# Kernel tuning notes

Hardware: AMD Instinct MI355X
Metric: run time of the kernel (lower is better)

## Reference

```python
import jax, jax.numpy as jnp
import numpy as np

STATE_DIM, ACTION_DIM, HIDDEN_DIM = 12, 4, 16  # hidden_dim must equal state_dim+action_dim
LN_EPS = 1e-5


def setup_inputs() -> dict:
    key = jax.random.key(0)
    ks = jax.random.split(key, 12)
    B, T = 8192, 256
    D = STATE_DIM + ACTION_DIM  # 16
    H = HIDDEN_DIM
    s = 1.0 / np.sqrt(D)
    sh = 1.0 / np.sqrt(H)
    return {
        "initial_state": jax.random.normal(ks[0], (B, 1, STATE_DIM), jnp.float32),
        "commands": jax.random.normal(ks[1], (B, T, ACTION_DIM), jnp.float32),
        "ln_gamma": jnp.ones((D,), jnp.float32),
        "ln_beta": jnp.zeros((D,), jnp.float32),
        "W_in": jax.random.uniform(ks[2], (H, D), jnp.float32, -s, s),
        "b_in": jax.random.uniform(ks[3], (H,), jnp.float32, -s, s),
        "W_ih": jax.random.uniform(ks[4], (4 * H, D), jnp.float32, -sh, sh),  # LSTM input_size = D
        "W_hh": jax.random.uniform(ks[5], (4 * H, H), jnp.float32, -sh, sh),
        "b_ih": jax.random.uniform(ks[6], (4 * H,), jnp.float32, -sh, sh),
        "b_hh": jax.random.uniform(ks[7], (4 * H,), jnp.float32, -sh, sh),
        "W_out": jax.random.uniform(ks[8], (STATE_DIM, H), jnp.float32, -sh, sh),
        "b_out": jax.random.uniform(ks[9], (STATE_DIM,), jnp.float32, -sh, sh),
    }


def _normalize_sincos(state, cos_idx, sin_idx):
    sn, cs = state[:, sin_idx], state[:, cos_idx]
    norm = jnp.sqrt(sn * sn + cs * cs) + 1e-8
    return state.at[:, sin_idx].set(sn / norm).at[:, cos_idx].set(cs / norm)


def _forward(initial_state, commands, ln_gamma, ln_beta, W_in, b_in,
             W_ih, W_hh, b_ih, b_hh, W_out, b_out):
    B = initial_state.shape[0]
    H = W_hh.shape[1]
    state0 = initial_state[:, 0, :]  # (B, S)
    h0 = jnp.zeros((B, H), initial_state.dtype)
    c0 = jnp.zeros((B, H), initial_state.dtype)

    def step(carry, cmd_t):
        state, h, c = carry
        x = jnp.concatenate([state, cmd_t], axis=-1)          # (B, D)
        mu = jnp.mean(x, axis=-1, keepdims=True)
        var = jnp.mean((x - mu) ** 2, axis=-1, keepdims=True)
        x = (x - mu) * jax.lax.rsqrt(var + LN_EPS) * ln_gamma + ln_beta
        x = x @ W_in.T + b_in                                  # (B, H)
        gates = x @ W_ih.T + b_ih + h @ W_hh.T + b_hh          # (B, 4H)
        i, f, g, o = jnp.split(gates, 4, axis=-1)
        c = jax.nn.sigmoid(f) * c + jax.nn.sigmoid(i) * jnp.tanh(g)
        h = jax.nn.sigmoid(o) * jnp.tanh(c)
        state = state + h @ W_out.T + b_out                    # (B, S)
        state = _normalize_sincos(state, 1, 2)
        state = _normalize_sincos(state, 3, 4)
        state = _normalize_sincos(state, 5, 6)
        return (state, h, c), state

    _, outs = jax.lax.scan(step, (state0, h0, c0), jnp.swapaxes(commands, 0, 1))
    return jnp.swapaxes(outs, 0, 1)  # (B, T, S)


def reference(initial_state, commands, ln_gamma, ln_beta, W_in, b_in,
              W_ih, W_hh, b_ih, b_hh, W_out, b_out):
    return _forward(initial_state, commands, ln_gamma, ln_beta, W_in, b_in,
                    W_ih, W_hh, b_ih, b_hh, W_out, b_out)
```

## Files before the change

kernel.cpp:

```cpp
#include <hip/hip_runtime.h>

typedef float f32x2 __attribute__((ext_vector_type(2)));
typedef float f32x4 __attribute__((ext_vector_type(4)));
typedef _Float16 h16x2 __attribute__((ext_vector_type(2)));
typedef __fp16 fp16x2_raw __attribute__((ext_vector_type(2)));

#define LOG2E 1.44269504088896340736f

static __device__ __forceinline__ float rcp_fast(float x) { return __builtin_amdgcn_rcpf(x); }

static __device__ __forceinline__ f32x2 mk2(float a, float b) { f32x2 v; v[0] = a; v[1] = b; return v; }

static __device__ __forceinline__ float sigmoid_fast(float x) {
    return rcp_fast(1.0f + __builtin_amdgcn_exp2f(-LOG2E * x));
}

static __device__ __forceinline__ float tanh_fast(float x) {
    float a = __builtin_fabsf(x);
    float t = __builtin_amdgcn_exp2f(-2.0f * LOG2E * a);
    float r = (1.0f - t) * rcp_fast(1.0f + t);
    return __builtin_copysignf(r, x);
}

static __device__ __forceinline__ float fdot2(h16x2 a, h16x2 b, float c) {
#if __has_builtin(__builtin_amdgcn_fdot2)
    return __builtin_amdgcn_fdot2(a, b, c, false);
#else
    return c + (float)(a[0]) * (float)(b[0]) + (float)(a[1]) * (float)(b[1]);
#endif
}

static __device__ __forceinline__ h16x2 pk(float a, float b) {
    fp16x2_raw r = __builtin_amdgcn_cvt_pkrtz(a, b);
    return __builtin_bit_cast(h16x2, r);
}

static __device__ __forceinline__ void load_pairs16(const float* p, f32x2* dst) {
    const f32x4* q4 = (const f32x4*)p;
    f32x4 a = q4[0], b = q4[1], c = q4[2], d = q4[3];
    dst[0] = __builtin_shufflevector(a, a, 0, 1);
    dst[1] = __builtin_shufflevector(a, a, 2, 3);
    dst[2] = __builtin_shufflevector(b, b, 0, 1);
    dst[3] = __builtin_shufflevector(b, b, 2, 3);
    dst[4] = __builtin_shufflevector(c, c, 0, 1);
    dst[5] = __builtin_shufflevector(c, c, 2, 3);
    dst[6] = __builtin_shufflevector(d, d, 0, 1);
    dst[7] = __builtin_shufflevector(d, d, 2, 3);
}

__global__ __launch_bounds__(64, 2) void vm_kernel(
    const float* __restrict__ init_state,
    const float* __restrict__ commands,
    const float* __restrict__ ln_g,
    const float* __restrict__ ln_b,
    const float* __restrict__ W_in,
    const float* __restrict__ b_in,
    const float* __restrict__ W_ih,
    const float* __restrict__ W_hh,
    const float* __restrict__ b_ih,
    const float* __restrict__ b_hh,
    const float* __restrict__ W_out,
    const float* __restrict__ b_out,
    float* __restrict__ out,
    int B, int T)
{
    const int lane = threadIdx.x;
    const int j = lane & 15;
    const int g = lane >> 4;
    const int b = blockIdx.x * 4 + g;
    const int gbase = (lane & 48) << 2;
    const bool is_state = (j < 12);

    f32x2 Wih[4][8], Wh32[4][8];
#pragma unroll
    for (int q = 0; q < 4; ++q) {
        load_pairs16(W_ih + (q * 16 + j) * 16, Wih[q]);
        load_pairs16(W_hh + (q * 16 + j) * 16, Wh32[q]);
    }

    f32x2 Wgx[4][8];
    float binacc[4];
#pragma unroll
    for (int q = 0; q < 4; ++q) {
        binacc[q] = 0.0f;
#pragma unroll
        for (int k2 = 0; k2 < 8; ++k2) Wgx[q][k2] = mk2(0.0f, 0.0f);
    }
#pragma unroll
    for (int m = 0; m < 16; ++m) {
        f32x2 wm[8];
        load_pairs16(W_in + m * 16, wm);
        float bm = b_in[m];
#pragma unroll
        for (int q = 0; q < 4; ++q) {
            float wim = Wih[q][m >> 1][m & 1];
            f32x2 w2 = mk2(wim, wim);
#pragma unroll
            for (int k2 = 0; k2 < 8; ++k2) Wgx[q][k2] += w2 * wm[k2];
            binacc[q] += wim * bm;
        }
    }
    float sg[4], cst[4];
    {
        f32x2 gg2[8], bt2[8];
        load_pairs16(ln_g, gg2);
        load_pairs16(ln_b, bt2);
#pragma unroll
        for (int q = 0; q < 4; ++q) {
            f32x2 ss = mk2(0.0f, 0.0f), cc = mk2(0.0f, 0.0f);
#pragma unroll
            for (int k2 = 0; k2 < 8; ++k2) {
                cc += Wgx[q][k2] * bt2[k2];
                Wgx[q][k2] *= gg2[k2];
                ss += Wgx[q][k2];
            }
            sg[q]  = ss[0] + ss[1];
            cst[q] = cc[0] + cc[1] + binacc[q] + b_ih[q * 16 + j] + b_hh[q * 16 + j];
        }
    }

    h16x2 WgxH[4][8], WhH[4][8];
#pragma unroll
    for (int q = 0; q < 4; ++q)
#pragma unroll
        for (int k2 = 0; k2 < 8; ++k2) {
            WgxH[q][k2] = pk(Wgx[q][k2][0], Wgx[q][k2][1]);
            WhH[q][k2]  = pk(Wh32[q][k2][0], Wh32[q][k2][1]);
        }

    h16x2 WoH[8];
    float bo = 0.0f;
#pragma unroll
    for (int k2 = 0; k2 < 8; ++k2) WoH[k2] = pk(0.0f, 0.0f);
    if (is_state) {
        f32x2 wo32[8];
        load_pairs16(W_out + j * 16, wo32);
#pragma unroll
        for (int k2 = 0; k2 < 8; ++k2) WoH[k2] = pk(wo32[k2][0], wo32[k2][1]);
        bo = b_out[j];
    }

    const h16x2 one2 = pk(1.0f, 1.0f);

    float st = is_state ? init_state[b * 12 + j] : 0.0f;
    float c = 0.0f;
    h16x2 hpk[8];
#pragma unroll
    for (int k2 = 0; k2 < 8; ++k2) hpk[k2] = pk(0.0f, 0.0f);

    const float* cmd_ptr = commands + (size_t)b * T * 4 + (j >= 12 ? j - 12 : 0);
    float* out_ptr = out + (size_t)b * T * 12 + j;
    const bool do_cmd = (j >= 12);

    int pj = j;
    if (j >= 1 && j <= 6) pj = ((j - 1) ^ 1) + 1;
    const int paddr = ((lane & 48) | pj) << 2;
    const bool donorm = (j >= 1 && j <= 6);

#define GATHER16(v, dst)                                                      \
    do {                                                                      \
        int _s = __float_as_int(v);                                           \
        _Pragma("unroll")                                                     \
        for (int _i = 0; _i < 16; ++_i)                                       \
            dst[_i] = __int_as_float(                                         \
                __builtin_amdgcn_ds_bpermute(gbase + (_i << 2), _s));         \
    } while (0)

    float cmd0 = do_cmd ? cmd_ptr[0] : 0.0f;
    h16x2 xpk[8];
    float mu, inv;
    {
        float xv = is_state ? st : cmd0;
        float xg[16];
        GATHER16(xv, xg);
#pragma unroll
        for (int i = 0; i < 8; ++i) xpk[i] = pk(xg[2 * i], xg[2 * i + 1]);
        float s0 = 0.0f, s1 = 0.0f, q0 = 0.0f, q1 = 0.0f;
#pragma unroll
        for (int i = 0; i < 4; ++i) {
            s0 = fdot2(xpk[i], one2, s0);
            s1 = fdot2(xpk[i + 4], one2, s1);
            q0 = fdot2(xpk[i], xpk[i], q0);
            q1 = fdot2(xpk[i + 4], xpk[i + 4], q1);
        }
        mu = (s0 + s1) * 0.0625f;
        float var = (q0 + q1) * 0.0625f - mu * mu;
        inv = __builtin_amdgcn_rsqf(var + 1e-5f);
    }

    float cmdS = do_cmd ? cmd_ptr[(size_t)(T > 1 ? 1 : 0) * 4] : 0.0f;
    float cmdN = do_cmd ? cmd_ptr[(size_t)(T > 2 ? 2 : 0) * 4] : 0.0f;

    for (int t = 0; t < T; ++t) {
        float gx[4], gh[4];
#pragma unroll
        for (int q = 0; q < 4; ++q) {
            float a0 = 0.0f, a1 = 0.0f, h0 = 0.0f, h1 = 0.0f;
#pragma unroll
            for (int k = 0; k < 4; ++k) {
                a0 = fdot2(WgxH[q][k], xpk[k], a0);
                a1 = fdot2(WgxH[q][k + 4], xpk[k + 4], a1);
                h0 = fdot2(WhH[q][k], hpk[k], h0);
                h1 = fdot2(WhH[q][k + 4], hpk[k + 4], h1);
            }
            gx[q] = a0 + a1;
            gh[q] = h0 + h1;
        }
        float nmi = -mu * inv;
        float gi = __builtin_fmaf(gx[0], inv, __builtin_fmaf(nmi, sg[0], cst[0] + gh[0]));
        float gf = __builtin_fmaf(gx[1], inv, __builtin_fmaf(nmi, sg[1], cst[1] + gh[1]));
        float gG = __builtin_fmaf(gx[2], inv, __builtin_fmaf(nmi, sg[2], cst[2] + gh[2]));
        float go = __builtin_fmaf(gx[3], inv, __builtin_fmaf(nmi, sg[3], cst[3] + gh[3]));

        float iv = sigmoid_fast(gi);
        float fv = sigmoid_fast(gf);
        float gv = tanh_fast(gG);
        float ov = sigmoid_fast(go);
        c = fv * c + iv * gv;
        float hv = ov * tanh_fast(c);

        {
            float hg[16];
            GATHER16(hv, hg);
#pragma unroll
            for (int i = 0; i < 8; ++i) hpk[i] = pk(hg[2 * i], hg[2 * i + 1]);
        }

        float o0 = 0.0f, o1 = 0.0f;
#pragma unroll
        for (int k = 0; k < 4; ++k) {
            o0 = fdot2(WoH[k], hpk[k], o0);
            o1 = fdot2(WoH[k + 4], hpk[k + 4], o1);
        }
        float st_raw = st + (o0 + o1) + bo;

        float pv = __int_as_float(
            __builtin_amdgcn_ds_bpermute(paddr, __float_as_int(st_raw)));
        float nrm = __builtin_amdgcn_sqrtf(st_raw * st_raw + pv * pv) + 1e-8f;
        float stn = st_raw * rcp_fast(nrm);
        st = donorm ? stn : st_raw;
        if (is_state) out_ptr[0] = st;
        out_ptr += 12;

        {
            float xv = is_state ? st : cmdS;
            float xg[16];
            GATHER16(xv, xg);
#pragma unroll
            for (int i = 0; i < 8; ++i) xpk[i] = pk(xg[2 * i], xg[2 * i + 1]);
        }
        float s0 = 0.0f, s1 = 0.0f, q0 = 0.0f, q1 = 0.0f;
#pragma unroll
        for (int i = 0; i < 4; ++i) {
            s0 = fdot2(xpk[i], one2, s0);
            s1 = fdot2(xpk[i + 4], one2, s1);
            q0 = fdot2(xpk[i], xpk[i], q0);
            q1 = fdot2(xpk[i + 4], xpk[i + 4], q1);
        }
        mu = (s0 + s1) * 0.0625f;
        float var = (q0 + q1) * 0.0625f - mu * mu;
        inv = __builtin_amdgcn_rsqf(var + 1e-5f);

        cmdS = cmdN;
        int tn = t + 3;
        if (tn > T - 1) tn = T - 1;
        if (do_cmd) cmdN = cmd_ptr[(size_t)tn * 4];
    }
#undef GATHER16
}

extern "C" void kernel_launch(void* const* d_in, const int* in_sizes, int n_in,
                              void* d_out, int out_size, void* d_ws, size_t ws_size,
                              hipStream_t stream) {
    const float* init_state = (const float*)d_in[0];
    const float* commands   = (const float*)d_in[1];
    const float* ln_g       = (const float*)d_in[2];
    const float* ln_b       = (const float*)d_in[3];
    const float* W_in       = (const float*)d_in[4];
    const float* b_in       = (const float*)d_in[5];
    const float* W_ih       = (const float*)d_in[6];
    const float* W_hh       = (const float*)d_in[7];
    const float* b_ih       = (const float*)d_in[8];
    const float* b_hh       = (const float*)d_in[9];
    const float* W_out      = (const float*)d_in[10];
    const float* b_out      = (const float*)d_in[11];

    int B = in_sizes[0] / 12;
    int T = in_sizes[1] / (B * 4);

    int blocks = B / 4;
    vm_kernel<<<blocks, 64, 0, stream>>>(init_state, commands, ln_g, ln_b,
                                         W_in, b_in, W_ih, W_hh, b_ih, b_hh,
                                         W_out, b_out, (float*)d_out, B, T);
}
```

Before: 393.1 us.

## Replicate state update across lanes to drop second per-step gather

```diff
diff --git a/kernel.cpp b/kernel.cpp
--- a/kernel.cpp
+++ b/kernel.cpp
@@ -48,7 +48,7 @@
     dst[7] = __builtin_shufflevector(d, d, 2, 3);
 }
 
-__global__ __launch_bounds__(64, 2) void vm_kernel(
+__global__ __launch_bounds__(64, 1) void vm_kernel(
     const float* __restrict__ init_state,
     const float* __restrict__ commands,
     const float* __restrict__ ln_g,
@@ -69,7 +69,6 @@
     const int g = lane >> 4;
     const int b = blockIdx.x * 4 + g;
     const int gbase = (lane & 48) << 2;
-    const bool is_state = (j < 12);
 
     f32x2 Wih[4][8], Wh32[4][8];
 #pragma unroll
@@ -128,34 +127,35 @@
             WhH[q][k2]  = pk(Wh32[q][k2][0], Wh32[q][k2][1]);
         }
 
-    h16x2 WoH[8];
-    float bo = 0.0f;
-#pragma unroll
-    for (int k2 = 0; k2 < 8; ++k2) WoH[k2] = pk(0.0f, 0.0f);
-    if (is_state) {
+    h16x2 WoF[12][8];
+    float boF[12];
+#pragma unroll
+    for (int i = 0; i < 12; ++i) {
         f32x2 wo32[8];
-        load_pairs16(W_out + j * 16, wo32);
-#pragma unroll
-        for (int k2 = 0; k2 < 8; ++k2) WoH[k2] = pk(wo32[k2][0], wo32[k2][1]);
-        bo = b_out[j];
+        load_pairs16(W_out + i * 16, wo32);
+#pragma unroll
+        for (int k2 = 0; k2 < 8; ++k2) WoF[i][k2] = pk(wo32[k2][0], wo32[k2][1]);
+        boF[i] = b_out[i];
     }
 
     const h16x2 one2 = pk(1.0f, 1.0f);
 
-    float st = is_state ? init_state[b * 12 + j] : 0.0f;
+    float st[12];
+    {
+        const f32x4* isp = (const f32x4*)(init_state + b * 12);
+        f32x4 s0 = isp[0], s1 = isp[1], s2 = isp[2];
+#pragma unroll
+        for (int i = 0; i < 4; ++i) {
+            st[i] = s0[i]; st[4 + i] = s1[i]; st[8 + i] = s2[i];
+        }
+    }
     float c = 0.0f;
     h16x2 hpk[8];
 #pragma unroll
     for (int k2 = 0; k2 < 8; ++k2) hpk[k2] = pk(0.0f, 0.0f);
 
-    const float* cmd_ptr = commands + (size_t)b * T * 4 + (j >= 12 ? j - 12 : 0);
-    float* out_ptr = out + (size_t)b * T * 12 + j;
-    const bool do_cmd = (j >= 12);
-
-    int pj = j;
-    if (j >= 1 && j <= 6) pj = ((j - 1) ^ 1) + 1;
-    const int paddr = ((lane & 48) | pj) << 2;
-    const bool donorm = (j >= 1 && j <= 6);
+    const f32x4* cmd4 = (const f32x4*)(commands + (size_t)b * T * 4);
+    float* outp = out + (size_t)b * T * 12 + j * 4;
 
 #define GATHER16(v, dst)                                                      \
     do {                                                                      \
@@ -166,15 +166,19 @@
                 __builtin_amdgcn_ds_bpermute(gbase + (_i << 2), _s));         \
     } while (0)
 
-    float cmd0 = do_cmd ? cmd_ptr[0] : 0.0f;
+#define PACK_X(xpk, cv)                                                       \
+    do {                                                                      \
+        xpk[0] = pk(st[0], st[1]);  xpk[1] = pk(st[2], st[3]);                \
+        xpk[2] = pk(st[4], st[5]);  xpk[3] = pk(st[6], st[7]);                \
+        xpk[4] = pk(st[8], st[9]);  xpk[5] = pk(st[10], st[11]);              \
+        xpk[6] = pk(cv[0], cv[1]);  xpk[7] = pk(cv[2], cv[3]);                \
+    } while (0)
+
     h16x2 xpk[8];
     float mu, inv;
     {
-        float xv = is_state ? st : cmd0;
-        float xg[16];
-        GATHER16(xv, xg);
-#pragma unroll
-        for (int i = 0; i < 8; ++i) xpk[i] = pk(xg[2 * i], xg[2 * i + 1]);
+        f32x4 cmd0 = cmd4[0];
+        PACK_X(xpk, cmd0);
         float s0 = 0.0f, s1 = 0.0f, q0 = 0.0f, q1 = 0.0f;
 #pragma unroll
         for (int i = 0; i < 4; ++i) {
@@ -188,8 +192,8 @@
         inv = __builtin_amdgcn_rsqf(var + 1e-5f);
     }
 
-    float cmdS = do_cmd ? cmd_ptr[(size_t)(T > 1 ? 1 : 0) * 4] : 0.0f;
-    float cmdN = do_cmd ? cmd_ptr[(size_t)(T > 2 ? 2 : 0) * 4] : 0.0f;
+    f32x4 cmdS = cmd4[T > 1 ? 1 : 0];
+    f32x4 cmdN = cmd4[T > 2 ? 2 : 0];
 
     for (int t = 0; t < T; ++t) {
         float gx[4], gh[4];
@@ -226,29 +230,35 @@
             for (int i = 0; i < 8; ++i) hpk[i] = pk(hg[2 * i], hg[2 * i + 1]);
         }
 
-        float o0 = 0.0f, o1 = 0.0f;
-#pragma unroll
-        for (int k = 0; k < 4; ++k) {
-            o0 = fdot2(WoH[k], hpk[k], o0);
-            o1 = fdot2(WoH[k + 4], hpk[k + 4], o1);
-        }
-        float st_raw = st + (o0 + o1) + bo;
-
-        float pv = __int_as_float(
-            __builtin_amdgcn_ds_bpermute(paddr, __float_as_int(st_raw)));
-        float nrm = __builtin_amdgcn_sqrtf(st_raw * st_raw + pv * pv) + 1e-8f;
-        float stn = st_raw * rcp_fast(nrm);
-        st = donorm ? stn : st_raw;
-        if (is_state) out_ptr[0] = st;
-        out_ptr += 12;
+#pragma unroll
+        for (int i = 0; i < 12; ++i) {
+            float d0 = 0.0f, d1 = 0.0f;
+#pragma unroll
+            for (int k = 0; k < 4; ++k) {
+                d0 = fdot2(WoF[i][k], hpk[k], d0);
+                d1 = fdot2(WoF[i][k + 4], hpk[k + 4], d1);
+            }
+            st[i] = st[i] + (d0 + d1) + boF[i];
+        }
+
+#pragma unroll
+        for (int p = 0; p < 3; ++p) {
+            float a = st[1 + 2 * p], bq = st[2 + 2 * p];
+            float r = rcp_fast(__builtin_amdgcn_sqrtf(a * a + bq * bq) + 1e-8f);
+            st[1 + 2 * p] = a * r; st[2 + 2 * p] = bq * r;
+        }
 
         {
-            float xv = is_state ? st : cmdS;
-            float xg[16];
-            GATHER16(xv, xg);
-#pragma unroll
-            for (int i = 0; i < 8; ++i) xpk[i] = pk(xg[2 * i], xg[2 * i + 1]);
-        }
+            f32x4 v0, v1, v2;
+#pragma unroll
+            for (int i = 0; i < 4; ++i) { v0[i] = st[i]; v1[i] = st[4 + i]; v2[i] = st[8 + i]; }
+            f32x4 w = (j == 1) ? v1 : v0;
+            w = (j == 2) ? v2 : w;
+            if (j < 3) *(f32x4*)outp = w;
+            outp += 12;
+        }
+
+        PACK_X(xpk, cmdS);
         float s0 = 0.0f, s1 = 0.0f, q0 = 0.0f, q1 = 0.0f;
 #pragma unroll
         for (int i = 0; i < 4; ++i) {
@@ -264,9 +274,10 @@
         cmdS = cmdN;
         int tn = t + 3;
         if (tn > T - 1) tn = T - 1;
-        if (do_cmd) cmdN = cmd_ptr[(size_t)tn * 4];
+        cmdN = cmd4[tn];
     }
 #undef GATHER16
+#undef PACK_X
 }
 
 extern "C" void kernel_launch(void* const* d_in, const int* in_sizes, int n_in,
```

After: 502.0 us. 27.7% more time.

## Interleave two independent LSTM recurrences per lane and pack hidden-state gathers

Applied to the files above, without the earlier changes.

```diff
diff --git a/kernel.cpp b/kernel.cpp
--- a/kernel.cpp
+++ b/kernel.cpp
@@ -33,6 +33,11 @@
 static __device__ __forceinline__ h16x2 pk(float a, float b) {
     fp16x2_raw r = __builtin_amdgcn_cvt_pkrtz(a, b);
     return __builtin_bit_cast(h16x2, r);
+}
+
+template <int CTRL>
+static __device__ __forceinline__ int dppi(int src) {
+    return __builtin_amdgcn_update_dpp(0, src, CTRL, 0xF, 0xF, true);
 }
 
 static __device__ __forceinline__ void load_pairs16(const float* p, f32x2* dst) {
@@ -48,7 +53,7 @@
     dst[7] = __builtin_shufflevector(d, d, 2, 3);
 }
 
-__global__ __launch_bounds__(64, 2) void vm_kernel(
+__global__ __launch_bounds__(64, 1) void vm_kernel(
     const float* __restrict__ init_state,
     const float* __restrict__ commands,
     const float* __restrict__ ln_g,
@@ -67,9 +72,11 @@
     const int lane = threadIdx.x;
     const int j = lane & 15;
     const int g = lane >> 4;
-    const int b = blockIdx.x * 4 + g;
     const int gbase = (lane & 48) << 2;
     const bool is_state = (j < 12);
+    const int bbase = blockIdx.x * 4;
+    const int bA = bbase + (g & 1);
+    const int bB = bbase + 2 + (g & 1);
 
     f32x2 Wih[4][8], Wh32[4][8];
 #pragma unroll
@@ -140,133 +147,166 @@
         bo = b_out[j];
     }
 
+#define PINH(x) do { int _t = __builtin_bit_cast(int, x); \
+    asm volatile("" : "+v"(_t)); x = __builtin_bit_cast(h16x2, _t); } while (0)
+#define PINF(x) asm volatile("" : "+v"(x))
+#pragma unroll
+    for (int q = 0; q < 4; ++q) {
+#pragma unroll
+        for (int k2 = 0; k2 < 8; ++k2) { PINH(WgxH[q][k2]); PINH(WhH[q][k2]); }
+        PINF(sg[q]); PINF(cst[q]);
+    }
+#pragma unroll
+    for (int k2 = 0; k2 < 8; ++k2) PINH(WoH[k2]);
+    PINF(bo);
+
     const h16x2 one2 = pk(1.0f, 1.0f);
-
-    float st = is_state ? init_state[b * 12 + j] : 0.0f;
-    float c = 0.0f;
-    h16x2 hpk[8];
-#pragma unroll
-    for (int k2 = 0; k2 < 8; ++k2) hpk[k2] = pk(0.0f, 0.0f);
-
-    const float* cmd_ptr = commands + (size_t)b * T * 4 + (j >= 12 ? j - 12 : 0);
-    float* out_ptr = out + (size_t)b * T * 12 + j;
-    const bool do_cmd = (j >= 12);
 
     int pj = j;
     if (j >= 1 && j <= 6) pj = ((j - 1) ^ 1) + 1;
     const int paddr = ((lane & 48) | pj) << 2;
     const bool donorm = (j >= 1 && j <= 6);
 
-#define GATHER16(v, dst)                                                      \
-    do {                                                                      \
-        int _s = __float_as_int(v);                                           \
-        _Pragma("unroll")                                                     \
-        for (int _i = 0; _i < 16; ++_i)                                       \
-            dst[_i] = __int_as_float(                                         \
-                __builtin_amdgcn_ds_bpermute(gbase + (_i << 2), _s));         \
-    } while (0)
-
-    float cmd0 = do_cmd ? cmd_ptr[0] : 0.0f;
-    h16x2 xpk[8];
-    float mu, inv;
-    {
-        float xv = is_state ? st : cmd0;
-        float xg[16];
-        GATHER16(xv, xg);
-#pragma unroll
-        for (int i = 0; i < 8; ++i) xpk[i] = pk(xg[2 * i], xg[2 * i + 1]);
-        float s0 = 0.0f, s1 = 0.0f, q0 = 0.0f, q1 = 0.0f;
-#pragma unroll
-        for (int i = 0; i < 4; ++i) {
-            s0 = fdot2(xpk[i], one2, s0);
-            s1 = fdot2(xpk[i + 4], one2, s1);
-            q0 = fdot2(xpk[i], xpk[i], q0);
-            q1 = fdot2(xpk[i + 4], xpk[i + 4], q1);
-        }
-        mu = (s0 + s1) * 0.0625f;
-        float var = (q0 + q1) * 0.0625f - mu * mu;
-        inv = __builtin_amdgcn_rsqf(var + 1e-5f);
-    }
-
-    float cmdS = do_cmd ? cmd_ptr[(size_t)(T > 1 ? 1 : 0) * 4] : 0.0f;
-    float cmdN = do_cmd ? cmd_ptr[(size_t)(T > 2 ? 2 : 0) * 4] : 0.0f;
+    h16x2 xpkA[8], hpkA[8], xpkB[8], hpkB[8];
+    float stA, cA, muA, invA, cmdSA, cmdNA;
+    float stB, cB, muB, invB, cmdSB, cmdNB;
+    const float* cmdpA = commands + (size_t)bA * T * 4 + (j >= 12 ? j - 12 : 0);
+    const float* cmdpB = commands + (size_t)bB * T * 4 + (j >= 12 ? j - 12 : 0);
+    float* outpA = out + (size_t)bA * T * 12 + j;
+    float* outpB = out + (size_t)bB * T * 12 + j;
+
+#define GATHPK(v, dstpk)                                                      \
+    do {                                                                      \
+        int _own = __float_as_int(v);                                         \
+        int _par = dppi<0xB1>(_own);                                          \
+        h16x2 _pp = pk(v, __int_as_float(_par));                              \
+        int _ppi = __builtin_bit_cast(int, _pp);                              \
+        _Pragma("unroll")                                                     \
+        for (int _i = 0; _i < 8; ++_i)                                        \
+            dstpk[_i] = __builtin_bit_cast(h16x2,                             \
+                __builtin_amdgcn_ds_bpermute(gbase + (_i << 3), _ppi));       \
+    } while (0)
+
+#define PH_LN(S)                                                              \
+    do {                                                                      \
+        float _s0 = 0.f, _s1 = 0.f, _q0 = 0.f, _q1 = 0.f;                     \
+        _Pragma("unroll")                                                     \
+        for (int _i = 0; _i < 4; ++_i) {                                      \
+            _s0 = fdot2(xpk##S[_i], one2, _s0);                               \
+            _s1 = fdot2(xpk##S[_i + 4], one2, _s1);                           \
+            _q0 = fdot2(xpk##S[_i], xpk##S[_i], _q0);                         \
+            _q1 = fdot2(xpk##S[_i + 4], xpk##S[_i + 4], _q1);                 \
+        }                                                                     \
+        mu##S = (_s0 + _s1) * 0.0625f;                                        \
+        float _var = (_q0 + _q1) * 0.0625f - mu##S * mu##S;                   \
+        inv##S = __builtin_amdgcn_rsqf(_var + 1e-5f);                         \
+    } while (0)
+
+#define PH_GATES(S)                                                           \
+    float hv##S;                                                              \
+    do {                                                                      \
+        float _gx0 = 0.f, _gx1 = 0.f, _gx2 = 0.f, _gx3 = 0.f;                 \
+        float _gh0 = 0.f, _gh1 = 0.f, _gh2 = 0.f, _gh3 = 0.f;                 \
+        _Pragma("unroll")                                                     \
+        for (int _k = 0; _k < 8; ++_k) {                                      \
+            _gx0 = fdot2(WgxH[0][_k], xpk##S[_k], _gx0);                      \
+            _gx1 = fdot2(WgxH[1][_k], xpk##S[_k], _gx1);                      \
+            _gx2 = fdot2(WgxH[2][_k], xpk##S[_k], _gx2);                      \
+            _gx3 = fdot2(WgxH[3][_k], xpk##S[_k], _gx3);                      \
+            _gh0 = fdot2(WhH[0][_k], hpk##S[_k], _gh0);                       \
+            _gh1 = fdot2(WhH[1][_k], hpk##S[_k], _gh1);                       \
+            _gh2 = fdot2(WhH[2][_k], hpk##S[_k], _gh2);                       \
+            _gh3 = fdot2(WhH[3][_k], hpk##S[_k], _gh3);                       \
+        }                                                                     \
+        float _nmi = -mu##S * inv##S;                                         \
+        float _gi = __builtin_fmaf(_gx0, inv##S, __builtin_fmaf(_nmi, sg[0], cst[0] + _gh0)); \
+        float _gf = __builtin_fmaf(_gx1, inv##S, __builtin_fmaf(_nmi, sg[1], cst[1] + _gh1)); \
+        float _gG = __builtin_fmaf(_gx2, inv##S, __builtin_fmaf(_nmi, sg[2], cst[2] + _gh2)); \
+        float _go = __builtin_fmaf(_gx3, inv##S, __builtin_fmaf(_nmi, sg[3], cst[3] + _gh3)); \
+        float _iv = sigmoid_fast(_gi);                                        \
+        float _fv = sigmoid_fast(_gf);                                        \
+        float _gv = tanh_fast(_gG);                                           \
+        float _ov = sigmoid_fast(_go);                                        \
+        c##S = _fv * c##S + _iv * _gv;                                        \
+        hv##S = _ov * tanh_fast(c##S);                                        \
+    } while (0)
+
+#define PH_WOUT(S, STPRED)                                                    \
+    do {                                                                      \
+        float _o0 = 0.f, _o1 = 0.f;                                           \
+        _Pragma("unroll")                                                     \
+        for (int _k = 0; _k < 4; ++_k) {                                      \
+            _o0 = fdot2(WoH[_k], hpk##S[_k], _o0);                            \
+            _o1 = fdot2(WoH[_k + 4], hpk##S[_k + 4], _o1);                    \
+        }                                                                     \
+        float _sraw = st##S + (_o0 + _o1) + bo;                               \
+        float _pv = __int_as_float(                                           \
+            __builtin_amdgcn_ds_bpermute(paddr, __float_as_int(_sraw)));      \
+        float _nrm = __builtin_amdgcn_sqrtf(_sraw * _sraw + _pv * _pv) + 1e-8f; \
+        float _stn = _sraw * rcp_fast(_nrm);                                  \
+        st##S = donorm ? _stn : _sraw;                                        \
+        if (STPRED) outp##S[0] = st##S;                                       \
+        outp##S += 12;                                                        \
+    } while (0)
+
+#define PH_XGATH(S)                                                           \
+    do {                                                                      \
+        float _xv = is_state ? st##S : cmdS##S;                               \
+        GATHPK(_xv, xpk##S);                                                  \
+    } while (0)
+
+#define PH_CMD(S, tt)                                                         \
+    do {                                                                      \
+        cmdS##S = cmdN##S;                                                    \
+        int _tn = (tt) + 3;                                                   \
+        if (_tn > T - 1) _tn = T - 1;                                         \
+        if (j >= 12) cmdN##S = cmdp##S[(size_t)_tn * 4];                      \
+    } while (0)
+
+#define INIT_STREAM(S, BS)                                                    \
+    do {                                                                      \
+        st##S = is_state ? init_state[(BS) * 12 + j] : 0.0f;                  \
+        c##S = 0.0f;                                                          \
+        _Pragma("unroll")                                                     \
+        for (int _k = 0; _k < 8; ++_k) hpk##S[_k] = pk(0.0f, 0.0f);           \
+        float _cmd0 = (j >= 12) ? cmdp##S[0] : 0.0f;                          \
+        float _xv = is_state ? st##S : _cmd0;                                 \
+        GATHPK(_xv, xpk##S);                                                  \
+        PH_LN(S);                                                             \
+        cmdS##S = (j >= 12) ? cmdp##S[(size_t)(T > 1 ? 1 : 0) * 4] : 0.0f;    \
+        cmdN##S = (j >= 12) ? cmdp##S[(size_t)(T > 2 ? 2 : 0) * 4] : 0.0f;    \
+    } while (0)
+
+    INIT_STREAM(A, bA);
+    INIT_STREAM(B, bB);
+
+    const bool predA = (lane < 32) && is_state;
+    const bool predB = (lane >= 32) && is_state;
 
     for (int t = 0; t < T; ++t) {
-        float gx[4], gh[4];
-#pragma unroll
-        for (int q = 0; q < 4; ++q) {
-            float a0 = 0.0f, a1 = 0.0f, h0 = 0.0f, h1 = 0.0f;
-#pragma unroll
-            for (int k = 0; k < 4; ++k) {
-                a0 = fdot2(WgxH[q][k], xpk[k], a0);
-                a1 = fdot2(WgxH[q][k + 4], xpk[k + 4], a1);
-                h0 = fdot2(WhH[q][k], hpk[k], h0);
-                h1 = fdot2(WhH[q][k + 4], hpk[k + 4], h1);
-            }
-            gx[q] = a0 + a1;
-            gh[q] = h0 + h1;
-        }
-        float nmi = -mu * inv;
-        float gi = __builtin_fmaf(gx[0], inv, __builtin_fmaf(nmi, sg[0], cst[0] + gh[0]));
-        float gf = __builtin_fmaf(gx[1], inv, __builtin_fmaf(nmi, sg[1], cst[1] + gh[1]));
-        float gG = __builtin_fmaf(gx[2], inv, __builtin_fmaf(nmi, sg[2], cst[2] + gh[2]));
-        float go = __builtin_fmaf(gx[3], inv, __builtin_fmaf(nmi, sg[3], cst[3] + gh[3]));
-
-        float iv = sigmoid_fast(gi);
-        float fv = sigmoid_fast(gf);
-        float gv = tanh_fast(gG);
-        float ov = sigmoid_fast(go);
-        c = fv * c + iv * gv;
-        float hv = ov * tanh_fast(c);
-
-        {
-            float hg[16];
-            GATHER16(hv, hg);
-#pragma unroll
-            for (int i = 0; i < 8; ++i) hpk[i] = pk(hg[2 * i], hg[2 * i + 1]);
-        }
-
-        float o0 = 0.0f, o1 = 0.0f;
-#pragma unroll
-        for (int k = 0; k < 4; ++k) {
-            o0 = fdot2(WoH[k], hpk[k], o0);
-            o1 = fdot2(WoH[k + 4], hpk[k + 4], o1);
-        }
-        float st_raw = st + (o0 + o1) + bo;
-
-        float pv = __int_as_float(
-            __builtin_amdgcn_ds_bpermute(paddr, __float_as_int(st_raw)));
-        float nrm = __builtin_amdgcn_sqrtf(st_raw * st_raw + pv * pv) + 1e-8f;
-        float stn = st_raw * rcp_fast(nrm);
-        st = donorm ? stn : st_raw;
-        if (is_state) out_ptr[0] = st;
-        out_ptr += 12;
-
-        {
-            float xv = is_state ? st : cmdS;
-            float xg[16];
-            GATHER16(xv, xg);
-#pragma unroll
-            for (int i = 0; i < 8; ++i) xpk[i] = pk(xg[2 * i], xg[2 * i + 1]);
-        }
-        float s0 = 0.0f, s1 = 0.0f, q0 = 0.0f, q1 = 0.0f;
-#pragma unroll
-        for (int i = 0; i < 4; ++i) {
-            s0 = fdot2(xpk[i], one2, s0);
-            s1 = fdot2(xpk[i + 4], one2, s1);
-            q0 = fdot2(xpk[i], xpk[i], q0);
-            q1 = fdot2(xpk[i + 4], xpk[i + 4], q1);
-        }
-        mu = (s0 + s1) * 0.0625f;
-        float var = (q0 + q1) * 0.0625f - mu * mu;
-        inv = __builtin_amdgcn_rsqf(var + 1e-5f);
-
-        cmdS = cmdN;
-        int tn = t + 3;
-        if (tn > T - 1) tn = T - 1;
-        if (do_cmd) cmdN = cmd_ptr[(size_t)tn * 4];
-    }
-#undef GATHER16
+        PH_GATES(A);
+        PH_GATES(B);
+        GATHPK(hvA, hpkA);
+        GATHPK(hvB, hpkB);
+        PH_WOUT(A, predA);
+        PH_WOUT(B, predB);
+        PH_XGATH(A);
+        PH_XGATH(B);
+        PH_LN(A);
+        PH_LN(B);
+        PH_CMD(A, t);
+        PH_CMD(B, t);
+    }
+
+#undef PINH
+#undef PINF
+#undef GATHPK
+#undef PH_LN
+#undef PH_GATES
+#undef PH_WOUT
+#undef PH_XGATH
+#undef PH_CMD
+#undef INIT_STREAM
 }
 
 extern "C" void kernel_launch(void* const* d_in, const int* in_sizes, int n_in,
```

Result: slower. 546.4 us (+39.0%).
